# Kernel tuning notes

Measured on AMD Instinct MI355X. Metric: run time of the kernel, lower is better.

Reference implementation:

```python
import jax, jax.numpy as jnp
import numpy as np

B, S, HID = 2, 2048, 2048
H = 16
HD = HID // H            # 128
HD2 = HD // 2            # 64 (rope dim per head)
LAT = HID // 8           # 256 latent dim
BASE = 10000.0


def _rotary_table(seq_len):
    # inv_freq over rope dim HD2
    inv_freq = 1.0 / (BASE ** (jnp.arange(0, HD2, 2, dtype=jnp.float32) / HD2))  # [HD2//2]
    pos = jnp.arange(seq_len, dtype=jnp.float32)
    sincos = pos[:, None] * inv_freq[None, :]                 # [S, HD2//2]
    return jnp.concatenate([jnp.sin(sincos), jnp.cos(sincos)], axis=-1)  # [S, HD2]


def _apply_rope(x, emb):
    # x: [B, S, H, HD2]; emb: [S, HD2]
    half = HD2 // 2
    x1, x2 = x[..., :half], x[..., half:]
    sin = emb[None, :, None, :half]
    cos = emb[None, :, None, half:]
    return jnp.concatenate([x1 * cos - x2 * sin, x1 * sin + x2 * cos], axis=-1)


def setup_inputs() -> dict:
    key = jax.random.key(0)
    ks = jax.random.split(key, 9)
    s = 0.02
    return {
        "hidden_states": jax.random.normal(ks[0], (B, S, HID), jnp.float32),
        "w_kv_d": jax.random.normal(ks[1], (HID, LAT), jnp.float32) * s,
        "w_q_d": jax.random.normal(ks[2], (HID, LAT), jnp.float32) * s,
        "w_k_u": jax.random.normal(ks[3], (LAT, H * HD2), jnp.float32) * s,
        "w_q_u": jax.random.normal(ks[4], (LAT, H * HD2), jnp.float32) * s,
        "w_v_u": jax.random.normal(ks[5], (LAT, H * HD), jnp.float32) * s,
        "w_rope_k": jax.random.normal(ks[6], (HID, HID // 2), jnp.float32) * s,
        "w_rope_q": jax.random.normal(ks[7], (LAT, HID // 2), jnp.float32) * s,
        "w_o": jax.random.normal(ks[8], (HID, HID), jnp.float32) * s,
    }


def reference(hidden_states, w_kv_d, w_q_d, w_k_u, w_q_u, w_v_u, w_rope_k, w_rope_q, w_o):
    b, s, _ = hidden_states.shape
    kv_d = hidden_states @ w_kv_d            # [B,S,LAT]
    q_d = hidden_states @ w_q_d              # [B,S,LAT]
    k_p = (kv_d @ w_k_u).reshape(b, s, H, HD2)
    q_p = (q_d @ w_q_u).reshape(b, s, H, HD2)
    v = (kv_d @ w_v_u).reshape(b, s, H, HD)
    k_r = (hidden_states @ w_rope_k).reshape(b, s, H, HD2)
    q_r = (q_d @ w_rope_q).reshape(b, s, H, HD2)

    emb = _rotary_table(s)
    k_r = _apply_rope(k_r, emb)
    q_r = _apply_rope(q_r, emb)

    k = jnp.concatenate([k_p, k_r], axis=-1)  # [B,S,H,HD]
    q = jnp.concatenate([q_p, q_r], axis=-1)

    scores = jnp.einsum('bqhd,bkhd->bhqk', q, k) / jnp.sqrt(jnp.float32(HD))
    causal = jnp.tril(jnp.ones((s, s), dtype=bool))
    scores = jnp.where(causal[None, None], scores, jnp.float32(-1e9))
    probs = jax.nn.softmax(scores, axis=-1)
    out = jnp.einsum('bhqk,bkhd->bqhd', probs, v).reshape(b, s, HID)
    return out @ w_o
```

## Files before the change

### kernel.cpp

```cpp
#include <hip/hip_runtime.h>
#include <hip/hip_bf16.h>

#define BB 2
#define SS 2048
#define HID 2048
#define NH 16
#define BS (BB*SS)
#define SCALE 0.088388347648318447f

typedef __bf16 bf16x8 __attribute__((ext_vector_type(8)));
typedef float f32x4 __attribute__((ext_vector_type(4)));

__device__ __forceinline__ bf16x8 ld_frag(const __hip_bfloat16* p) {
    uint4 u = *reinterpret_cast<const uint4*>(p);
    return __builtin_bit_cast(bf16x8, u);
}
__device__ __forceinline__ void store_c(__hip_bfloat16* C, size_t idx, float v) {
    C[idx] = __float2bfloat16(v);
}
__device__ __forceinline__ void store_c(float* C, size_t idx, float v) {
    C[idx] = v;
}
__device__ __forceinline__ ushort bf_bits(float v) {
    __hip_bfloat16 h = __float2bfloat16(v);
    return *reinterpret_cast<ushort*>(&h);
}

#define GLD16(gp, lp) \
  __builtin_amdgcn_global_load_lds((const __attribute__((address_space(1))) void*)(gp), \
                                   (__attribute__((address_space(3))) void*)(lp), 16, 0, 0)

__global__ __launch_bounds__(256) void convert_kernel(
    const float* __restrict__ src, __hip_bfloat16* __restrict__ dst, int n8)
{
    int i = blockIdx.x * blockDim.x + threadIdx.x;
    if (i >= n8) return;
    float4 a = reinterpret_cast<const float4*>(src)[2 * i];
    float4 b = reinterpret_cast<const float4*>(src)[2 * i + 1];
    ushort u[8] = { bf_bits(a.x), bf_bits(a.y), bf_bits(a.z), bf_bits(a.w),
                    bf_bits(b.x), bf_bits(b.y), bf_bits(b.z), bf_bits(b.w) };
    reinterpret_cast<uint4*>(dst)[i] = *reinterpret_cast<uint4*>(u);
}

__global__ __launch_bounds__(256) void transpose_weights_kernel(
    const float* s0, const float* s1, const float* s2, const float* s3,
    const float* s4, const float* s5, const float* s6, const float* s7,
    __hip_bfloat16* WT1, __hip_bfloat16* WT2, __hip_bfloat16* WT3,
    __hip_bfloat16* WTo)
{
    const float* srcs[8] = { s0, s1, s2, s3, s4, s5, s6, s7 };
    const int Rs[8] = { 2048, 2048, 2048, 256, 256, 256, 256, 2048 };
    const int Cs[8] = { 256, 256, 1024, 1024, 2048, 1024, 1024, 2048 };
    __hip_bfloat16* dsts[8] = {
        WT1, WT1 + (size_t)256 * 2048, WT1 + (size_t)512 * 2048,
        WT2, WT2 + (size_t)1024 * 256,
        WT3, WT3 + (size_t)1024 * 256,
        WTo };
    const int prefix[9] = { 0, 512, 1024, 3072, 3328, 3840, 4096, 4352, 8448 };

    int bid = blockIdx.x;
    int seg = 0;
    #pragma unroll
    for (int i = 0; i < 8; i++) if (bid >= prefix[i + 1]) seg = i + 1;
    int local = bid - prefix[seg];
    int R = Rs[seg], C = Cs[seg];
    int tilesC = C / 32;
    int tr = local / tilesC, tc = local % tilesC;
    int r0 = tr * 32, c0 = tc * 32;
    const float* src = srcs[seg];
    __hip_bfloat16* dst = dsts[seg];

    __shared__ float Ts[32][33];
    int t = threadIdx.x;
    int ty = t >> 5, tx = t & 31;
    #pragma unroll
    for (int k = 0; k < 4; k++) {
        int r = ty + k * 8;
        Ts[r][tx] = src[(size_t)(r0 + r) * C + c0 + tx];
    }
    __syncthreads();
    #pragma unroll
    for (int k = 0; k < 4; k++) {
        int r = ty + k * 8;
        dst[(size_t)(c0 + r) * R + r0 + tx] = __float2bfloat16(Ts[tx][r]);
    }
}

template <typename TC>
__global__ __launch_bounds__(256) void gemm_bt_kernel(
    const __hip_bfloat16* __restrict__ A, int lda,
    const __hip_bfloat16* __restrict__ Bt,
    TC* __restrict__ C0, int ldc0, int sp0, int off0, float cm0,
    TC* __restrict__ C1, int ldc1, int sp1, int off1, float cm1,
    int splitN, int K)
{
    __shared__ alignas(16) __hip_bfloat16 As[128 * 32];
    __shared__ alignas(16) __hip_bfloat16 Bs[128 * 32];

    const int bn = blockIdx.x * 128;
    const int bm = blockIdx.y * 128;
    const int t = threadIdx.x;
    const int w = t >> 6;
    const int lane = t & 63;
    const int l15 = lane & 15;
    const int quad = lane >> 4;
    const int wm = (w & 1) * 64;
    const int wn = (w >> 1) * 64;

    const int srow = lane >> 2;
    const int skcol = (lane & 3) * 8;

    f32x4 acc[4][4] = {};

    for (int k0 = 0; k0 < K; k0 += 32) {
        __syncthreads();
        #pragma unroll
        for (int i = 0; i < 2; i++) {
            int r = w * 32 + i * 16 + srow;
            GLD16(A + (size_t)(bm + r) * lda + k0 + skcol, &As[r * 32 + skcol]);
            GLD16(Bt + (size_t)(bn + r) * K + k0 + skcol, &Bs[r * 32 + skcol]);
        }
        __syncthreads();

        bf16x8 af[4], bf[4];
        #pragma unroll
        for (int mt = 0; mt < 4; mt++)
            af[mt] = ld_frag(&As[(wm + mt * 16 + l15) * 32 + quad * 8]);
        #pragma unroll
        for (int nt = 0; nt < 4; nt++)
            bf[nt] = ld_frag(&Bs[(wn + nt * 16 + l15) * 32 + quad * 8]);
        #pragma unroll
        for (int mt = 0; mt < 4; mt++)
            #pragma unroll
            for (int nt = 0; nt < 4; nt++)
                acc[mt][nt] = __builtin_amdgcn_mfma_f32_16x16x32_bf16(
                    af[mt], bf[nt], acc[mt][nt], 0, 0, 0);
    }

    #pragma unroll
    for (int nt = 0; nt < 4; nt++) {
        int col = bn + wn + nt * 16 + l15;
        TC* Cp; int c, ld, s64, off; float cm;
        if (col < splitN) { Cp = C0; c = col; ld = ldc0; s64 = sp0; off = off0; cm = cm0; }
        else { Cp = C1; c = col - splitN; ld = ldc1; s64 = sp1; off = off1; cm = cm1; }
        if (s64 == 2) {
            #pragma unroll
            for (int mt = 0; mt < 4; mt++) {
                int row0 = bm + wm + mt * 16 + quad * 4;
                #pragma unroll
                for (int r = 0; r < 4; r++)
                    store_c(Cp, (size_t)c * 4096 + row0 + r, acc[mt][nt][r] * cm);
            }
        } else {
            int oc = s64 ? ((c >> 6) * 128 + (c & 63) + off) : c;
            #pragma unroll
            for (int mt = 0; mt < 4; mt++) {
                #pragma unroll
                for (int r = 0; r < 4; r++) {
                    int row = bm + wm + mt * 16 + quad * 4 + r;
                    store_c(Cp, (size_t)row * ld + oc, acc[mt][nt][r] * cm);
                }
            }
        }
    }
}

__global__ __launch_bounds__(256) void rope_kernel(
    __hip_bfloat16* __restrict__ Kb, __hip_bfloat16* __restrict__ Qb)
{
    int idx = blockIdx.x * blockDim.x + threadIdx.x;
    if (idx >= BS * NH * 32) return;
    int i = idx & 31;
    int h = (idx >> 5) & 15;
    int row = idx >> 9;
    int s = row & (SS - 1);

    float inv = exp2f(-(float)i * 0.4152410118609203f);
    float ang = (float)s * inv;
    float sn = sinf(ang), cs = cosf(ang);

    size_t obase = (size_t)row * 2048 + h * 128 + 64 + i;
    {
        float x1 = __bfloat162float(Kb[obase]);
        float x2 = __bfloat162float(Kb[obase + 32]);
        Kb[obase]      = __float2bfloat16(x1 * cs - x2 * sn);
        Kb[obase + 32] = __float2bfloat16(x1 * sn + x2 * cs);
    }
    {
        float x1 = __bfloat162float(Qb[obase]);
        float x2 = __bfloat162float(Qb[obase + 32]);
        Qb[obase]      = __float2bfloat16(x1 * cs - x2 * sn);
        Qb[obase + 32] = __float2bfloat16(x1 * sn + x2 * cs);
    }
}

__global__ __launch_bounds__(256) void flash_attn_kernel(
    const __hip_bfloat16* __restrict__ Q,
    const __hip_bfloat16* __restrict__ Kb,
    const __hip_bfloat16* __restrict__ Vt,
    __hip_bfloat16* __restrict__ O)
{
    __shared__ alignas(16) __hip_bfloat16 Kt[4 * 64 * 32];
    __shared__ alignas(16) __hip_bfloat16 Vs[2 * 128 * 32];
    __shared__ alignas(16) __hip_bfloat16 Sp[4][32 * 72];

    const int bxq = (gridDim.x - 1) - blockIdx.x;
    const int h = blockIdx.y;
    const int b = blockIdx.z;
    const int t = threadIdx.x;
    const int w = t >> 6;
    const int lane = t & 63;
    const int l15 = lane & 15;
    const int quad = lane >> 4;
    const int qbase = bxq * 128;

    const __hip_bfloat16* Kbase = Kb + (size_t)(b * SS) * 2048 + h * 128;
    const __hip_bfloat16* Vtb = Vt + (size_t)(h * 128) * 4096 + b * SS;

    bf16x8 qf[2][4];
    #pragma unroll
    for (int qs = 0; qs < 2; qs++) {
        const __hip_bfloat16* qrow =
            Q + (size_t)(b * SS + qbase + w * 32 + qs * 16 + l15) * 2048 + h * 128;
        #pragma unroll
        for (int ds = 0; ds < 4; ds++)
            qf[qs][ds] = ld_frag(qrow + ds * 32 + quad * 8);
    }

    float m_i[2] = { -INFINITY, -INFINITY };
    float l_i[2] = { 0.0f, 0.0f };
    f32x4 acc[2][8] = {};

    const int Lr = lane >> 2;
    const int Lc = (lane & 3) ^ ((lane >> 3) & 3);
    const int rsl = (l15 >> 1) & 3;
    const int kvh_w = w >> 1, dh_w = w & 1;
    const int ntiles = 2 * bxq + 2;

    for (int kt = 0; kt < ntiles; kt++) {
        const int kvbase = kt * 64;
        __syncthreads();

        #pragma unroll
        for (int i = 0; i < 4; i++) {
            GLD16(Kbase + (size_t)(kvbase + i * 16 + Lr) * 2048 + w * 32 + Lc * 8,
                  &Kt[w * 2048 + i * 512 + lane * 8]);
        }
        #pragma unroll
        for (int i = 0; i < 4; i++) {
            GLD16(Vtb + (size_t)(dh_w * 64 + i * 16 + Lr) * 4096
                      + kvbase + kvh_w * 32 + Lc * 8,
                  &Vs[kvh_w * 4096 + dh_w * 2048 + i * 512 + lane * 8]);
        }
        __syncthreads();

        f32x4 st[4][2];
        #pragma unroll
        for (int kvsub = 0; kvsub < 4; kvsub++) {
            st[kvsub][0] = f32x4{};
            st[kvsub][1] = f32x4{};
            #pragma unroll
            for (int ds = 0; ds < 4; ds++) {
                bf16x8 kf = ld_frag(&Kt[ds * 2048 + (kvsub * 16 + l15) * 32
                                        + (quad ^ rsl) * 8]);
                #pragma unroll
                for (int qs = 0; qs < 2; qs++)
                    st[kvsub][qs] = __builtin_amdgcn_mfma_f32_16x16x32_bf16(
                        kf, qf[qs][ds], st[kvsub][qs], 0, 0, 0);
            }
        }
        #pragma unroll
        for (int qs = 0; qs < 2; qs++) {
            int q = qbase + w * 32 + qs * 16 + l15;
            #pragma unroll
            for (int kvsub = 0; kvsub < 4; kvsub++) {
                #pragma unroll
                for (int r = 0; r < 4; r++) {
                    int kv = kvbase + kvsub * 16 + quad * 4 + r;
                    st[kvsub][qs][r] = (kv <= q) ? st[kvsub][qs][r] * SCALE
                                                 : -INFINITY;
                }
            }
        }

        float alpha[2];
        #pragma unroll
        for (int qs = 0; qs < 2; qs++) {
            float tm = st[0][qs][0];
            #pragma unroll
            for (int kvsub = 0; kvsub < 4; kvsub++)
                #pragma unroll
                for (int r = 0; r < 4; r++) tm = fmaxf(tm, st[kvsub][qs][r]);
            tm = fmaxf(tm, __shfl_xor(tm, 16));
            tm = fmaxf(tm, __shfl_xor(tm, 32));
            float mnew = fmaxf(m_i[qs], tm);
            float rs = 0.0f;
            #pragma unroll
            for (int kvsub = 0; kvsub < 4; kvsub++)
                #pragma unroll
                for (int r = 0; r < 4; r++) {
                    float pv = __expf(st[kvsub][qs][r] - mnew);
                    st[kvsub][qs][r] = pv;
                    rs += pv;
                }
            rs += __shfl_xor(rs, 16);
            rs += __shfl_xor(rs, 32);
            alpha[qs] = __expf(m_i[qs] - mnew);
            m_i[qs] = mnew;
            l_i[qs] = l_i[qs] * alpha[qs] + rs;
        }

        #pragma unroll
        for (int qs = 0; qs < 2; qs++) {
            #pragma unroll
            for (int kvsub = 0; kvsub < 4; kvsub++) {
                ushort pk[4] = { bf_bits(st[kvsub][qs][0]), bf_bits(st[kvsub][qs][1]),
                                 bf_bits(st[kvsub][qs][2]), bf_bits(st[kvsub][qs][3]) };
                *reinterpret_cast<uint2*>(
                    &Sp[w][(qs * 16 + l15) * 72 + kvsub * 16 + quad * 4]) =
                    *reinterpret_cast<uint2*>(pk);
            }
        }

        #pragma unroll
        for (int qs = 0; qs < 2; qs++) {
            float al[4];
            #pragma unroll
            for (int r = 0; r < 4; r++) al[r] = __shfl(alpha[qs], quad * 4 + r, 64);
            #pragma unroll
            for (int dt = 0; dt < 8; dt++)
                #pragma unroll
                for (int r = 0; r < 4; r++) acc[qs][dt][r] *= al[r];
        }

        #pragma unroll
        for (int kvh = 0; kvh < 2; kvh++) {
            bf16x8 pf[2];
            #pragma unroll
            for (int qs = 0; qs < 2; qs++)
                pf[qs] = ld_frag(&Sp[w][(qs * 16 + l15) * 72 + kvh * 32 + quad * 8]);
            #pragma unroll
            for (int dt = 0; dt < 8; dt++) {
                bf16x8 vf = ld_frag(&Vs[kvh * 4096 + (dt * 16 + l15) * 32
                                        + (quad ^ rsl) * 8]);
                #pragma unroll
                for (int qs = 0; qs < 2; qs++)
                    acc[qs][dt] = __builtin_amdgcn_mfma_f32_16x16x32_bf16(
                        pf[qs], vf, acc[qs][dt], 0, 0, 0);
            }
        }
    }

    #pragma unroll
    for (int qs = 0; qs < 2; qs++) {
        float li[4];
        #pragma unroll
        for (int r = 0; r < 4; r++) li[r] = __shfl(l_i[qs], quad * 4 + r, 64);
        #pragma unroll
        for (int r = 0; r < 4; r++) {
            int row = qbase + w * 32 + qs * 16 + quad * 4 + r;
            __hip_bfloat16* orow = O + (size_t)(b * SS + row) * 2048 + h * 128;
            float inv_l = 1.0f / li[r];
            #pragma unroll
            for (int dt = 0; dt < 8; dt++)
                orow[dt * 16 + l15] = __float2bfloat16(acc[qs][dt][r] * inv_l);
        }
    }
}

extern "C" void kernel_launch(void* const* d_in, const int* in_sizes, int n_in,
                              void* d_out, int out_size, void* d_ws, size_t ws_size,
                              hipStream_t stream)
{
    const float* hs       = (const float*)d_in[0];
    const float* w_kv_d   = (const float*)d_in[1];
    const float* w_q_d    = (const float*)d_in[2];
    const float* w_k_u    = (const float*)d_in[3];
    const float* w_q_u    = (const float*)d_in[4];
    const float* w_v_u    = (const float*)d_in[5];
    const float* w_rope_k = (const float*)d_in[6];
    const float* w_rope_q = (const float*)d_in[7];
    const float* w_o      = (const float*)d_in[8];
    float* out = (float*)d_out;

    char* p = (char*)d_ws;
    auto alloc = [&](size_t nelem) {
        __hip_bfloat16* r = (__hip_bfloat16*)p;
        p += nelem * sizeof(__hip_bfloat16);
        return r;
    };
    __hip_bfloat16* hsb  = alloc((size_t)BS * HID);
    __hip_bfloat16* qkvd = alloc((size_t)BS * 512);
    __hip_bfloat16* WT1  = alloc((size_t)1536 * 2048);
    __hip_bfloat16* WT2  = alloc((size_t)3072 * 256);
    __hip_bfloat16* WT3  = alloc((size_t)2048 * 256);
    __hip_bfloat16* WTo  = alloc((size_t)2048 * 2048);
    __hip_bfloat16* Kbuf = alloc((size_t)BS * HID);
    __hip_bfloat16* Qbuf = alloc((size_t)BS * HID);
    __hip_bfloat16* Vtb  = alloc((size_t)HID * BS);
    __hip_bfloat16* attn = hsb;

    dim3 blk(256);

    convert_kernel<<<dim3((BS * HID / 8 + 255) / 256), blk, 0, stream>>>(
        hs, hsb, BS * HID / 8);
    transpose_weights_kernel<<<dim3(8448), blk, 0, stream>>>(
        w_kv_d, w_q_d, w_rope_k, w_k_u, w_v_u, w_q_u, w_rope_q, w_o,
        WT1, WT2, WT3, WTo);

    gemm_bt_kernel<__hip_bfloat16><<<dim3(1536 / 128, BS / 128), blk, 0, stream>>>(
        hsb, 2048, WT1,
        qkvd, 512, 0, 0, 1.0f,
        Kbuf, 2048, 1, 64, 1.0f,
        512, 2048);
    gemm_bt_kernel<__hip_bfloat16><<<dim3(3072 / 128, BS / 128), blk, 0, stream>>>(
        qkvd, 512, WT2,
        Kbuf, 2048, 1, 0, 1.0f,
        Vtb, 0, 2, 0, 1.0f,
        1024, 256);
    gemm_bt_kernel<__hip_bfloat16><<<dim3(2048 / 128, BS / 128), blk, 0, stream>>>(
        qkvd + 256, 512, WT3,
        Qbuf, 2048, 1, 0, 1.0f,
        Qbuf, 2048, 1, 64, 1.0f,
        1024, 256);
    rope_kernel<<<dim3((BS * NH * 32 + 255) / 256), blk, 0, stream>>>(Kbuf, Qbuf);
    flash_attn_kernel<<<dim3(SS / 128, NH, BB), blk, 0, stream>>>(
        Qbuf, Kbuf, Vtb, attn);
    gemm_bt_kernel<float><<<dim3(2048 / 128, BS / 128), blk, 0, stream>>>(
        attn, 2048, WTo,
        out, 2048, 0, 0, 1.0f,
        out, 2048, 0, 0, 1.0f,
        2048, 2048);
}
```

Baseline: 388.4 us.

## Rewrite flash attention with 32x32 MFMA, K double-buffering, register P and lazy rescale

The attention kernel switches from 16x16x32 to 32x32x16 bf16 MFMA and computes the transposed score tile so each lane owns one query row. The P matrix stays in registers and is rearranged with permlane32_swap instead of going through shared memory, and K tiles are double-buffered with prefetch and manual vmcnt waits. Softmax moves to exp2 with a folded scale, and the accumulator rescale is skipped when the running max grows by no more than a threshold. The hand-written waitcnt and barrier ordering is fragile, and the lazy-max threshold allows larger intermediate values.

```diff
diff --git a/kernel.cpp b/kernel.cpp
--- a/kernel.cpp
+++ b/kernel.cpp
@@ -7,9 +7,12 @@
 #define NH 16
 #define BS (BB*SS)
 #define SCALE 0.088388347648318447f
+#define C2LOG 0.12751743f
 
 typedef __bf16 bf16x8 __attribute__((ext_vector_type(8)));
 typedef float f32x4 __attribute__((ext_vector_type(4)));
+typedef float f32x16 __attribute__((ext_vector_type(16)));
+typedef unsigned int uintx2 __attribute__((ext_vector_type(2)));
 
 __device__ __forceinline__ bf16x8 ld_frag(const __hip_bfloat16* p) {
     uint4 u = *reinterpret_cast<const uint4*>(p);
@@ -200,9 +203,8 @@
     const __hip_bfloat16* __restrict__ Vt,
     __hip_bfloat16* __restrict__ O)
 {
-    __shared__ alignas(16) __hip_bfloat16 Kt[4 * 64 * 32];
+    __shared__ alignas(16) __hip_bfloat16 Ktd[2 * 4 * 64 * 32];
     __shared__ alignas(16) __hip_bfloat16 Vs[2 * 128 * 32];
-    __shared__ alignas(16) __hip_bfloat16 Sp[4][32 * 72];
 
     const int bxq = (gridDim.x - 1) - blockIdx.x;
     const int h = blockIdx.y;
@@ -210,162 +212,168 @@
     const int t = threadIdx.x;
     const int w = t >> 6;
     const int lane = t & 63;
-    const int l15 = lane & 15;
-    const int quad = lane >> 4;
+    const int l31 = lane & 31;
+    const int hi = lane >> 5;
+    const int swl = (l31 >> 1) & 3;
     const int qbase = bxq * 128;
+    const int q = qbase + w * 32 + l31;
 
     const __hip_bfloat16* Kbase = Kb + (size_t)(b * SS) * 2048 + h * 128;
     const __hip_bfloat16* Vtb = Vt + (size_t)(h * 128) * 4096 + b * SS;
 
-    bf16x8 qf[2][4];
-    #pragma unroll
-    for (int qs = 0; qs < 2; qs++) {
-        const __hip_bfloat16* qrow =
-            Q + (size_t)(b * SS + qbase + w * 32 + qs * 16 + l15) * 2048 + h * 128;
-        #pragma unroll
-        for (int ds = 0; ds < 4; ds++)
-            qf[qs][ds] = ld_frag(qrow + ds * 32 + quad * 8);
-    }
-
-    float m_i[2] = { -INFINITY, -INFINITY };
-    float l_i[2] = { 0.0f, 0.0f };
-    f32x4 acc[2][8] = {};
+    bf16x8 qf[8];
+    {
+        const __hip_bfloat16* qrow = Q + (size_t)(b * SS + q) * 2048 + h * 128;
+        #pragma unroll
+        for (int s = 0; s < 8; s++)
+            qf[s] = ld_frag(qrow + s * 16 + hi * 8);
+    }
 
     const int Lr = lane >> 2;
     const int Lc = (lane & 3) ^ ((lane >> 3) & 3);
-    const int rsl = (l15 >> 1) & 3;
     const int kvh_w = w >> 1, dh_w = w & 1;
     const int ntiles = 2 * bxq + 2;
 
+    float m_i = -INFINITY;
+    float l_i = 0.0f;
+    f32x16 acc[4] = {};
+
+    #pragma unroll
+    for (int i = 0; i < 4; i++)
+        GLD16(Kbase + (size_t)(i * 16 + Lr) * 2048 + w * 32 + Lc * 8,
+              &Ktd[w * 2048 + i * 512 + lane * 8]);
+    asm volatile("" :: "v"(qf[0]), "v"(qf[1]), "v"(qf[2]), "v"(qf[3]),
+                       "v"(qf[4]), "v"(qf[5]), "v"(qf[6]), "v"(qf[7]));
+
     for (int kt = 0; kt < ntiles; kt++) {
-        const int kvbase = kt * 64;
-        __syncthreads();
-
-        #pragma unroll
-        for (int i = 0; i < 4; i++) {
-            GLD16(Kbase + (size_t)(kvbase + i * 16 + Lr) * 2048 + w * 32 + Lc * 8,
-                  &Kt[w * 2048 + i * 512 + lane * 8]);
-        }
-        #pragma unroll
-        for (int i = 0; i < 4; i++) {
+        const int kvb = kt * 64;
+        const int par = kt & 1;
+
+        __builtin_amdgcn_s_barrier();
+        asm volatile("" ::: "memory");
+
+        #pragma unroll
+        for (int i = 0; i < 4; i++)
             GLD16(Vtb + (size_t)(dh_w * 64 + i * 16 + Lr) * 4096
-                      + kvbase + kvh_w * 32 + Lc * 8,
+                      + kvb + kvh_w * 32 + Lc * 8,
                   &Vs[kvh_w * 4096 + dh_w * 2048 + i * 512 + lane * 8]);
-        }
-        __syncthreads();
-
-        f32x4 st[4][2];
-        #pragma unroll
-        for (int kvsub = 0; kvsub < 4; kvsub++) {
-            st[kvsub][0] = f32x4{};
-            st[kvsub][1] = f32x4{};
-            #pragma unroll
-            for (int ds = 0; ds < 4; ds++) {
-                bf16x8 kf = ld_frag(&Kt[ds * 2048 + (kvsub * 16 + l15) * 32
-                                        + (quad ^ rsl) * 8]);
-                #pragma unroll
-                for (int qs = 0; qs < 2; qs++)
-                    st[kvsub][qs] = __builtin_amdgcn_mfma_f32_16x16x32_bf16(
-                        kf, qf[qs][ds], st[kvsub][qs], 0, 0, 0);
-            }
-        }
-        #pragma unroll
-        for (int qs = 0; qs < 2; qs++) {
-            int q = qbase + w * 32 + qs * 16 + l15;
-            #pragma unroll
-            for (int kvsub = 0; kvsub < 4; kvsub++) {
+        {
+            const int kvb1 = ((kt + 1 < ntiles) ? kt + 1 : ntiles - 1) * 64;
+            __hip_bfloat16* kdst = &Ktd[((kt + 1) & 1) * 8192 + w * 2048];
+            #pragma unroll
+            for (int i = 0; i < 4; i++)
+                GLD16(Kbase + (size_t)(kvb1 + i * 16 + Lr) * 2048 + w * 32 + Lc * 8,
+                      kdst + i * 512 + lane * 8);
+        }
+        asm volatile("s_waitcnt vmcnt(8)" ::: "memory");
+        __builtin_amdgcn_s_barrier();
+        asm volatile("" ::: "memory");
+
+        const __hip_bfloat16* kb_base = &Ktd[par * 8192];
+        f32x16 st[2] = {};
+        #pragma unroll
+        for (int s = 0; s < 8; s++)
+            #pragma unroll
+            for (int kb = 0; kb < 2; kb++) {
+                bf16x8 kf = ld_frag(kb_base + (s >> 1) * 2048 + (kb * 32 + l31) * 32
+                                    + ((2 * (s & 1) + hi) ^ swl) * 8);
+                st[kb] = __builtin_amdgcn_mfma_f32_32x32x16_bf16(
+                    kf, qf[s], st[kb], 0, 0, 0);
+            }
+
+        const int thr = q - kvb - 4 * hi;
+        float tmx = -INFINITY;
+        #pragma unroll
+        for (int kb = 0; kb < 2; kb++)
+            #pragma unroll
+            for (int g = 0; g < 4; g++)
                 #pragma unroll
                 for (int r = 0; r < 4; r++) {
-                    int kv = kvbase + kvsub * 16 + quad * 4 + r;
-                    st[kvsub][qs][r] = (kv <= q) ? st[kvsub][qs][r] * SCALE
-                                                 : -INFINITY;
+                    const int e = g * 4 + r;
+                    float v = (kb * 32 + 8 * g + r <= thr) ? st[kb][e] : -INFINITY;
+                    st[kb][e] = v;
+                    tmx = fmaxf(tmx, v);
                 }
-            }
-        }
-
-        float alpha[2];
-        #pragma unroll
-        for (int qs = 0; qs < 2; qs++) {
-            float tm = st[0][qs][0];
-            #pragma unroll
-            for (int kvsub = 0; kvsub < 4; kvsub++)
+        tmx = fmaxf(tmx, __shfl_xor(tmx, 32));
+        const float m2x = tmx * C2LOG;
+
+        const bool nosc = __all(m2x <= m_i + 8.0f);
+        const float mnew = nosc ? m_i : fmaxf(m_i, m2x);
+        float rs = 0.0f;
+        #pragma unroll
+        for (int kb = 0; kb < 2; kb++)
+            #pragma unroll
+            for (int e = 0; e < 16; e++) {
+                float p = exp2f(fmaf(st[kb][e], C2LOG, -mnew));
+                st[kb][e] = p;
+                rs += p;
+            }
+        rs += __shfl_xor(rs, 32);
+        if (!nosc) {
+            const float alpha = exp2f(m_i - mnew);
+            m_i = mnew;
+            l_i *= alpha;
+            #pragma unroll
+            for (int dt = 0; dt < 4; dt++)
                 #pragma unroll
-                for (int r = 0; r < 4; r++) tm = fmaxf(tm, st[kvsub][qs][r]);
-            tm = fmaxf(tm, __shfl_xor(tm, 16));
-            tm = fmaxf(tm, __shfl_xor(tm, 32));
-            float mnew = fmaxf(m_i[qs], tm);
-            float rs = 0.0f;
-            #pragma unroll
-            for (int kvsub = 0; kvsub < 4; kvsub++)
+                for (int e = 0; e < 16; e++)
+                    acc[dt][e] *= alpha;
+        }
+        l_i += rs;
+
+        uint4 af[4];
+        #pragma unroll
+        for (int kb = 0; kb < 2; kb++) {
+            unsigned int pk[4][2];
+            #pragma unroll
+            for (int g = 0; g < 4; g++)
                 #pragma unroll
-                for (int r = 0; r < 4; r++) {
-                    float pv = __expf(st[kvsub][qs][r] - mnew);
-                    st[kvsub][qs][r] = pv;
-                    rs += pv;
+                for (int i = 0; i < 2; i++) {
+                    float2 fp = make_float2(st[kb][g * 4 + 2 * i],
+                                            st[kb][g * 4 + 2 * i + 1]);
+                    __hip_bfloat162 h2 = __float22bfloat162_rn(fp);
+                    pk[g][i] = *reinterpret_cast<unsigned int*>(&h2);
                 }
-            rs += __shfl_xor(rs, 16);
-            rs += __shfl_xor(rs, 32);
-            alpha[qs] = __expf(m_i[qs] - mnew);
-            m_i[qs] = mnew;
-            l_i[qs] = l_i[qs] * alpha[qs] + rs;
-        }
-
-        #pragma unroll
-        for (int qs = 0; qs < 2; qs++) {
-            #pragma unroll
-            for (int kvsub = 0; kvsub < 4; kvsub++) {
-                ushort pk[4] = { bf_bits(st[kvsub][qs][0]), bf_bits(st[kvsub][qs][1]),
-                                 bf_bits(st[kvsub][qs][2]), bf_bits(st[kvsub][qs][3]) };
-                *reinterpret_cast<uint2*>(
-                    &Sp[w][(qs * 16 + l15) * 72 + kvsub * 16 + quad * 4]) =
-                    *reinterpret_cast<uint2*>(pk);
-            }
-        }
-
-        #pragma unroll
-        for (int qs = 0; qs < 2; qs++) {
-            float al[4];
-            #pragma unroll
-            for (int r = 0; r < 4; r++) al[r] = __shfl(alpha[qs], quad * 4 + r, 64);
-            #pragma unroll
-            for (int dt = 0; dt < 8; dt++)
-                #pragma unroll
-                for (int r = 0; r < 4; r++) acc[qs][dt][r] *= al[r];
-        }
-
-        #pragma unroll
-        for (int kvh = 0; kvh < 2; kvh++) {
-            bf16x8 pf[2];
-            #pragma unroll
-            for (int qs = 0; qs < 2; qs++)
-                pf[qs] = ld_frag(&Sp[w][(qs * 16 + l15) * 72 + kvh * 32 + quad * 8]);
-            #pragma unroll
-            for (int dt = 0; dt < 8; dt++) {
-                bf16x8 vf = ld_frag(&Vs[kvh * 4096 + (dt * 16 + l15) * 32
-                                        + (quad ^ rsl) * 8]);
-                #pragma unroll
-                for (int qs = 0; qs < 2; qs++)
-                    acc[qs][dt] = __builtin_amdgcn_mfma_f32_16x16x32_bf16(
-                        pf[qs], vf, acc[qs][dt], 0, 0, 0);
-            }
-        }
-    }
-
-    #pragma unroll
-    for (int qs = 0; qs < 2; qs++) {
-        float li[4];
-        #pragma unroll
-        for (int r = 0; r < 4; r++) li[r] = __shfl(l_i[qs], quad * 4 + r, 64);
-        #pragma unroll
-        for (int r = 0; r < 4; r++) {
-            int row = qbase + w * 32 + qs * 16 + quad * 4 + r;
-            __hip_bfloat16* orow = O + (size_t)(b * SS + row) * 2048 + h * 128;
-            float inv_l = 1.0f / li[r];
-            #pragma unroll
-            for (int dt = 0; dt < 8; dt++)
-                orow[dt * 16 + l15] = __float2bfloat16(acc[qs][dt][r] * inv_l);
-        }
-    }
+            #pragma unroll
+            for (int sl = 0; sl < 2; sl++) {
+                uintx2 r0 = __builtin_amdgcn_permlane32_swap(
+                    pk[2 * sl][0], pk[2 * sl + 1][0], false, false);
+                uintx2 r1 = __builtin_amdgcn_permlane32_swap(
+                    pk[2 * sl][1], pk[2 * sl + 1][1], false, false);
+                af[kb * 2 + sl] = make_uint4(r0[0], r1[0], r0[1], r1[1]);
+            }
+        }
+
+        asm volatile("s_waitcnt vmcnt(4)" ::: "memory");
+        __builtin_amdgcn_s_barrier();
+        asm volatile("" ::: "memory");
+
+        #pragma unroll
+        for (int s = 0; s < 4; s++) {
+            bf16x8 pf = __builtin_bit_cast(bf16x8, af[s]);
+            #pragma unroll
+            for (int dt = 0; dt < 4; dt++) {
+                bf16x8 vf = ld_frag(&Vs[(s >> 1) * 4096 + (dt * 32 + l31) * 32
+                                        + ((2 * (s & 1) + hi) ^ swl) * 8]);
+                acc[dt] = __builtin_amdgcn_mfma_f32_32x32x16_bf16(
+                    vf, pf, acc[dt], 0, 0, 0);
+            }
+        }
+    }
+
+    const float inv_l = 1.0f / l_i;
+    __hip_bfloat16* orow = O + (size_t)(b * SS + q) * 2048 + h * 128;
+    #pragma unroll
+    for (int dt = 0; dt < 4; dt++)
+        #pragma unroll
+        for (int g = 0; g < 4; g++) {
+            ushort u[4];
+            #pragma unroll
+            for (int r = 0; r < 4; r++)
+                u[r] = bf_bits(acc[dt][g * 4 + r] * inv_l);
+            *reinterpret_cast<uint2*>(orow + dt * 32 + 8 * g + 4 * hi) =
+                *reinterpret_cast<uint2*>(u);
+        }
 }
 
 extern "C" void kernel_launch(void* const* d_in, const int* in_sizes, int n_in,
```

New measurement: 371.6 us. 4.3% less time.
